# Optimization experiments

Hardware: AMD Instinct MI355X
Metric: run time of the kernel (lower is better)

## Reference

```python
import jax, jax.numpy as jnp
import numpy as np

DIM = 1024
NUM_HEADS = 16
HEAD_DIM = DIM // NUM_HEADS
SCALE = HEAD_DIM ** -0.5


def setup_inputs() -> dict:
    key = jax.random.key(0)
    k1, k2, k3, k4, k5, k6 = jax.random.split(key, 6)
    B, S, L = 4, 8192, 512
    x = jax.random.normal(k1, (B, S, DIM), dtype=jnp.float32)
    latents = jax.random.normal(k2, (B, L, DIM), dtype=jnp.float32)
    # Linear weights stored torch-style as (out_features, in_features)
    w_q = jax.random.normal(k3, (DIM, DIM), dtype=jnp.float32) * (DIM ** -0.5)
    w_kv = jax.random.normal(k4, (2 * DIM, DIM), dtype=jnp.float32) * (DIM ** -0.5)
    w_out = jax.random.normal(k5, (DIM, DIM), dtype=jnp.float32) * (DIM ** -0.5)
    b_out = jax.random.normal(k6, (DIM,), dtype=jnp.float32) * 0.01
    return {"x": x, "latents": latents, "w_q": w_q, "w_kv": w_kv,
            "w_out": w_out, "b_out": b_out}


def reference(x, latents, w_q, w_kv, w_out, b_out):
    B, L, _ = latents.shape
    S = x.shape[1]
    q = latents @ w_q.T                      # (B, L, dim)
    kv = x @ w_kv.T                          # (B, S, 2*dim)
    k, v = jnp.split(kv, 2, axis=-1)         # each (B, S, dim)
    q = q.reshape(B, L, NUM_HEADS, HEAD_DIM)
    k = k.reshape(B, S, NUM_HEADS, HEAD_DIM)
    v = v.reshape(B, S, NUM_HEADS, HEAD_DIM)
    # attention scores: (B, H, L, S)
    attn = jnp.einsum('blhd,bshd->bhls', q, k) * SCALE
    attn = jax.nn.softmax(attn, axis=-1)
    out = jnp.einsum('bhls,bshd->blhd', attn, v)  # (B, L, H, D)
    out = out.reshape(B, L, DIM)
    return out @ w_out.T + b_out
```

## Files before the change

kernel.cpp:

```cpp
#include <hip/hip_runtime.h>
#include <hip/hip_bf16.h>
#include <cstdint>
#include <cstddef>

#define B_ 4
#define S_ 8192
#define L_ 512
#define DIM 1024
#define NUM_HEADS 16
#define HEAD_DIM 64
#define SCHUNK 4096
#define NSEG 2
#define SEGKEYS (SCHUNK / NSEG)
#define SCALE 0.125f
#define L2E 1.44269504088896f
#define F_SC (SCALE * L2E)

typedef __bf16 bf16;
typedef __bf16 bf16x8 __attribute__((ext_vector_type(8)));
typedef float f32x4 __attribute__((ext_vector_type(4)));

#define AS1 __attribute__((address_space(1)))
#define AS3 __attribute__((address_space(3)))
#define GLDS(g, l) __builtin_amdgcn_global_load_lds((const AS1 void*)(g), (AS3 void*)(l), 16, 0, 0)
#define LGKM_FENCE() asm volatile("s_waitcnt lgkmcnt(0)" ::: "memory")
#define MFMA16(a, b, c) __builtin_amdgcn_mfma_f32_16x16x32_bf16((a), (b), (c), 0, 0, 0)

__global__ void detect_dtype(const unsigned int* __restrict__ x, int* __restrict__ flag) {
  int lane = threadIdx.x;
  int cnt = 0;
  for (int i = 0; i < 4; ++i) {
    unsigned int w = x[lane * 4 + i];
    unsigned int e = (w >> 7) & 0xFFu;
    cnt += (e >= 117u && e <= 129u) ? 1 : 0;
  }
  cnt += __shfl_xor(cnt, 1);
  cnt += __shfl_xor(cnt, 2);
  cnt += __shfl_xor(cnt, 4);
  cnt += __shfl_xor(cnt, 8);
  cnt += __shfl_xor(cnt, 16);
  cnt += __shfl_xor(cnt, 32);
  if (lane == 0) *flag = (cnt < 128) ? 1 : 0;
}

template<int REMAP>
__global__ __launch_bounds__(256) void conv_bf16(
    const void* __restrict__ in, bf16* __restrict__ out, int nchunk, int srow0,
    const int* __restrict__ flagp)
{
  const bool f32in = (*flagp != 0);
  for (int c = blockIdx.x * 256 + threadIdx.x; c < nchunk; c += gridDim.x * 256) {
    size_t gc;
    if (REMAP) {
      int r = c >> 7, cc = c & 127;
      gc = ((size_t)((r >> 12) * 8192 + srow0 + (r & 4095)) << 7) + cc;
    } else {
      gc = (size_t)c;
    }
    if (f32in) {
      const f32x4* g = (const f32x4*)in + gc * 2;
      f32x4 lo = g[0], hi = g[1];
      bf16x8 w;
      w[0] = (bf16)lo[0]; w[1] = (bf16)lo[1]; w[2] = (bf16)lo[2]; w[3] = (bf16)lo[3];
      w[4] = (bf16)hi[0]; w[5] = (bf16)hi[1]; w[6] = (bf16)hi[2]; w[7] = (bf16)hi[3];
      *(bf16x8*)(out + (size_t)c * 8) = w;
    } else {
      *(bf16x8*)(out + (size_t)c * 8) = ((const bf16x8*)in)[gc];
    }
  }
}

template<int HAS_BIAS, int DUAL_OUT, int KV_SPLIT, int NBN>
__global__ __launch_bounds__(256) void gemm_nt(
    const bf16* __restrict__ Ap, const bf16* __restrict__ Bwp,
    void* __restrict__ Cp, void* __restrict__ C2p, const void* __restrict__ biasp,
    int M, int N, int K, const int* __restrict__ flagp)
{
  __shared__ __align__(16) bf16 lA[128 * 64];
  __shared__ __align__(16) bf16 lB[128 * 64];
  const int tid = threadIdx.x;
  const int lane = tid & 63, quad = lane >> 4, l16 = lane & 15, wave = tid >> 6;
  const int wm = wave >> 1, wn = wave & 1;
  const int f = blockIdx.x;
  const int xcd = f & 7, sidx = f >> 3;
  const int bn = sidx % NBN;
  const int bm = xcd * (M >> 10) + sidx / NBN;
  const bool f32in = (HAS_BIAS || DUAL_OUT) ? (*flagp != 0) : false;

  f32x4 acc[4][4] = {};
  const int nK = K >> 6;
  for (int kb = 0; kb < nK; ++kb) {
    __syncthreads();
#pragma unroll
    for (int i = 0; i < 4; ++i) {
      int e = i * 256 + tid;
      int row = e >> 3, cp = e & 7, gcp = cp ^ (row & 7);
      const bf16* ga = Ap + (size_t)(bm * 128 + row) * K + kb * 64 + gcp * 8;
      GLDS(ga, lA + e * 8);
      const bf16* gb = Bwp + (size_t)(bn * 128 + row) * K + kb * 64 + gcp * 8;
      GLDS(gb, lB + e * 8);
    }
    __syncthreads();

#pragma unroll
    for (int ks = 0; ks < 2; ++ks) {
      bf16x8 af[4], bfr[4];
#pragma unroll
      for (int t = 0; t < 4; ++t) {
        int rowA = wm * 64 + t * 16 + l16;
        int ca = (ks * 4 + quad) ^ (rowA & 7);
        af[t] = *(const bf16x8*)(lA + rowA * 64 + ca * 8);
        int rowB = wn * 64 + t * 16 + l16;
        int cb = (ks * 4 + quad) ^ (rowB & 7);
        bfr[t] = *(const bf16x8*)(lB + rowB * 64 + cb * 8);
      }
#pragma unroll
      for (int tm = 0; tm < 4; ++tm)
#pragma unroll
        for (int tn = 0; tn < 4; ++tn)
          acc[tm][tn] = MFMA16(af[tm], bfr[tn], acc[tm][tn]);
    }
  }

#pragma unroll
  for (int tn = 0; tn < 4; ++tn) {
    int col = bn * 128 + wn * 64 + tn * 16 + l16;
    float bv = 0.0f;
    if (HAS_BIAS)
      bv = f32in ? ((const float*)biasp)[col] : (float)((const bf16*)biasp)[col];
#pragma unroll
    for (int tm = 0; tm < 4; ++tm) {
#pragma unroll
      for (int r = 0; r < 4; ++r) {
        int rowc = bm * 128 + wm * 64 + tm * 16 + quad * 4 + r;
        float v = acc[tm][tn][r] + bv;
        if (KV_SPLIT) {
          if (col < 1024) ((bf16*)Cp)[(size_t)rowc * 1024 + col] = (bf16)v;
          else            ((bf16*)C2p)[(size_t)rowc * 1024 + col - 1024] = (bf16)v;
        } else if (DUAL_OUT && f32in) {
          ((float*)Cp)[(size_t)rowc * N + col] = v;
        } else {
          ((bf16*)Cp)[(size_t)rowc * N + col] = (bf16)v;
        }
      }
    }
  }
}

template<int FIRST>
__global__ __launch_bounds__(256) void attn_pass(
    const bf16* __restrict__ qb, const bf16* __restrict__ kc, const bf16* __restrict__ vc,
    float* __restrict__ Ost, float* __restrict__ lst)
{
  __shared__ __align__(16) bf16 lK[64 * 64];
  __shared__ __align__(16) bf16 lV[64][72];
  __shared__ __align__(16) bf16 pbuf[4][16][72];
  const int tid = threadIdx.x;
  const int lane = tid & 63, quad = lane >> 4, l16 = lane & 15, wave = tid >> 6;
  const int f = blockIdx.x;
  const int xcd = f & 7, sidx = f >> 3;
  const int lt = sidx & 7, ghi = sidx >> 3;
  const int g = ghi * 8 + xcd;
  const int h = g & 15, bs = g >> 4;
  const int b = bs >> 1, seg = bs & 1;
  const int l0 = lt * 64 + wave * 16;

  const bf16* qbase = qb + (size_t)(b * L_ + l0 + l16) * DIM + h * HEAD_DIM + quad * 8;
  bf16x8 qf0 = *(const bf16x8*)qbase;
  bf16x8 qf1 = *(const bf16x8*)(qbase + 32);

  f32x4 acc[4] = {};
  float lsum[4] = {0.0f, 0.0f, 0.0f, 0.0f};

  const int sbeg = seg * SEGKEYS;
  for (int s0 = sbeg; s0 < sbeg + SEGKEYS; s0 += 64) {
    __syncthreads();
    for (int i = 0; i < 2; ++i) {
      int e = i * 256 + tid;
      int row = e >> 3, cp = e & 7, gcp = cp ^ (row & 7);
      const bf16* gk = kc + (size_t)(b * SCHUNK + s0 + row) * DIM + h * HEAD_DIM + gcp * 8;
      GLDS(gk, lK + e * 8);
    }
    for (int i = 0; i < 2; ++i) {
      int e = i * 256 + tid;
      int row = e >> 3, cc = e & 7;
      bf16x8 vv = *(const bf16x8*)(vc + (size_t)(b * SCHUNK + s0 + row) * DIM + h * HEAD_DIM + cc * 8);
      int pg = (row >> 3) ^ cc;
#pragma unroll
      for (int j = 0; j < 8; ++j)
        lV[cc * 8 + j][pg * 8 + (row & 7)] = vv[j];
    }
    __syncthreads();

    f32x4 sc[4];
#pragma unroll
    for (int kt = 0; kt < 4; ++kt) {
      int rk = kt * 16 + l16;
      int p0c = quad ^ (rk & 7);
      int p1c = (4 + quad) ^ (rk & 7);
      bf16x8 kf0 = *(const bf16x8*)(lK + rk * 64 + p0c * 8);
      bf16x8 kf1 = *(const bf16x8*)(lK + rk * 64 + p1c * 8);
      f32x4 s4 = {};
      s4 = MFMA16(qf0, kf0, s4);
      s4 = MFMA16(qf1, kf1, s4);
      sc[kt] = s4;
    }

#pragma unroll
    for (int r = 0; r < 4; ++r) {
      float a0 = exp2f(fminf(sc[0][r] * F_SC, 40.0f));
      float a1 = exp2f(fminf(sc[1][r] * F_SC, 40.0f));
      float a2 = exp2f(fminf(sc[2][r] * F_SC, 40.0f));
      float a3 = exp2f(fminf(sc[3][r] * F_SC, 40.0f));
      lsum[r] += a0 + a1 + a2 + a3;
      pbuf[wave][quad * 4 + r][l16]      = (bf16)a0;
      pbuf[wave][quad * 4 + r][16 + l16] = (bf16)a1;
      pbuf[wave][quad * 4 + r][32 + l16] = (bf16)a2;
      pbuf[wave][quad * 4 + r][48 + l16] = (bf16)a3;
    }
    LGKM_FENCE();
#pragma unroll
    for (int half = 0; half < 2; ++half) {
      bf16x8 pf = *(const bf16x8*)&pbuf[wave][l16][half * 32 + quad * 8];
#pragma unroll
      for (int t4 = 0; t4 < 4; ++t4) {
        int c = t4 * 16 + l16;
        int pg = (half * 4 + quad) ^ (c >> 3);
        bf16x8 vf = *(const bf16x8*)&lV[c][pg * 8];
        acc[t4] = MFMA16(pf, vf, acc[t4]);
      }
    }
  }

#pragma unroll
  for (int r = 0; r < 4; ++r) {
    lsum[r] += __shfl_xor(lsum[r], 1, 16);
    lsum[r] += __shfl_xor(lsum[r], 2, 16);
    lsum[r] += __shfl_xor(lsum[r], 4, 16);
    lsum[r] += __shfl_xor(lsum[r], 8, 16);
  }

  float* Oseg = Ost + (size_t)seg * (B_ * L_ * DIM);
  float* lseg = lst + (size_t)seg * (B_ * NUM_HEADS * L_);
#pragma unroll
  for (int r = 0; r < 4; ++r) {
    int l = l0 + quad * 4 + r;
    if (l16 == 0) {
      int si = (b * NUM_HEADS + h) * L_ + l;
      if (FIRST) lseg[si] = lsum[r];
      else       lseg[si] += lsum[r];
    }
  }
#pragma unroll
  for (int t4 = 0; t4 < 4; ++t4)
#pragma unroll
    for (int r = 0; r < 4; ++r) {
      int l = l0 + quad * 4 + r;
      size_t oi = (size_t)(b * L_ + l) * DIM + h * HEAD_DIM + t4 * 16 + l16;
      if (FIRST) Oseg[oi] = acc[t4][r];
      else       Oseg[oi] += acc[t4][r];
    }
}

__global__ __launch_bounds__(256) void combine_kernel(
    const float* __restrict__ Ost, const float* __restrict__ lst, bf16* __restrict__ ao)
{
  int idx = (blockIdx.x * 256 + threadIdx.x) * 4;
  int d0 = idx & (DIM - 1);
  int row = idx >> 10;
  int b = row >> 9, l = row & (L_ - 1);
  int h = d0 >> 6;
  int si = (b * NUM_HEADS + h) * L_ + l;
  float lv = lst[si] + lst[B_ * NUM_HEADS * L_ + si];
  float linv = 1.0f / lv;
  f32x4 o0 = *(const f32x4*)(Ost + idx);
  f32x4 o1 = *(const f32x4*)(Ost + (size_t)(B_ * L_ * DIM) + idx);
#pragma unroll
  for (int j = 0; j < 4; ++j)
    ao[idx + j] = (bf16)((o0[j] + o1[j]) * linv);
}

extern "C" void kernel_launch(void* const* d_in, const int* in_sizes, int n_in,
                              void* d_out, int out_size, void* d_ws, size_t ws_size,
                              hipStream_t stream)
{
  (void)in_sizes; (void)n_in; (void)out_size; (void)ws_size;
  const void* x       = d_in[0];
  const void* latents = d_in[1];
  const void* w_q     = d_in[2];
  const void* w_kv    = d_in[3];
  const void* w_out   = d_in[4];
  const void* b_out   = d_in[5];

  char* ws = (char*)d_ws;
  int*   flag  = (int*)ws;
  bf16*  qb    = (bf16*)(ws + ((size_t)1   << 20));
  float* lst   = (float*)(ws + ((size_t)5  << 20));
  bf16*  ao    = (bf16*)(ws + ((size_t)6   << 20));
  float* Ost   = (float*)(ws + ((size_t)10 << 20));
  bf16*  kc    = (bf16*)(ws + ((size_t)26 << 20));
  bf16*  latb  = (bf16*)(ws + ((size_t)26 << 20));
  bf16*  wqb   = (bf16*)(ws + ((size_t)30 << 20));
  bf16*  vc    = (bf16*)(ws + ((size_t)58 << 20));
  bf16*  xcb   = (bf16*)(ws + ((size_t)90 << 20));
  bf16*  wkvb  = (bf16*)(ws + ((size_t)122 << 20));
  bf16*  woutb = (bf16*)(ws + ((size_t)122 << 20));

  detect_dtype<<<1, 64, 0, stream>>>((const unsigned int*)x, flag);

  const int Mx = B_ * SCHUNK;

  conv_bf16<0><<<1024, 256, 0, stream>>>(latents, latb, (B_ * L_ * DIM) / 8, 0, flag);
  conv_bf16<0><<<512,  256, 0, stream>>>(w_q, wqb, (DIM * DIM) / 8, 0, flag);
  conv_bf16<0><<<1024, 256, 0, stream>>>(w_kv, wkvb, (2 * DIM * DIM) / 8, 0, flag);

  gemm_nt<0, 0, 0, 8><<<128, 256, 0, stream>>>(
      latb, wqb, qb, nullptr, nullptr, B_ * L_, DIM, DIM, flag);

  conv_bf16<1><<<2048, 256, 0, stream>>>(x, xcb, (Mx * DIM) / 8, 0, flag);
  gemm_nt<0, 0, 1, 16><<<2048, 256, 0, stream>>>(
      xcb, wkvb, kc, vc, nullptr, Mx, 2048, DIM, flag);
  attn_pass<1><<<1024, 256, 0, stream>>>(qb, kc, vc, Ost, lst);

  conv_bf16<1><<<2048, 256, 0, stream>>>(x, xcb, (Mx * DIM) / 8, SCHUNK, flag);
  gemm_nt<0, 0, 1, 16><<<2048, 256, 0, stream>>>(
      xcb, wkvb, kc, vc, nullptr, Mx, 2048, DIM, flag);
  attn_pass<0><<<1024, 256, 0, stream>>>(qb, kc, vc, Ost, lst);

  conv_bf16<0><<<512, 256, 0, stream>>>(w_out, woutb, (DIM * DIM) / 8, 0, flag);
  combine_kernel<<<(B_ * L_ * DIM / 4) / 256, 256, 0, stream>>>(Ost, lst, ao);

  gemm_nt<1, 1, 0, 8><<<128, 256, 0, stream>>>(
      ao, woutb, d_out, nullptr, b_out, B_ * L_, DIM, DIM, flag);
}
```

Before: 612.8 us.

## Replace KV projection GEMM with 256x256 double-buffered pipelined kernel

Adds a dedicated KV-projection GEMM that uses 256x256 output tiles with 512 threads, double-buffered LDS staging through global_load_lds, interleaved prefetch of the next A and B tiles between MFMA phases, and raised wave priority around the MFMA bursts. It replaces the 128x128 single-buffered generic kernel for the two large x@w_kv^T launches and removes the KV_SPLIT path from the generic kernel. The aim is more data reuse per tile and load latency hidden behind compute. In exchange it uses more LDS and registers, which lowers occupancy, and it launches only 512 blocks.

```diff
diff --git a/kernel.cpp b/kernel.cpp
--- a/kernel.cpp
+++ b/kernel.cpp
@@ -24,6 +24,8 @@
 #define AS3 __attribute__((address_space(3)))
 #define GLDS(g, l) __builtin_amdgcn_global_load_lds((const AS1 void*)(g), (AS3 void*)(l), 16, 0, 0)
 #define LGKM_FENCE() asm volatile("s_waitcnt lgkmcnt(0)" ::: "memory")
+#define VMCNT4() asm volatile("s_waitcnt vmcnt(4)" ::: "memory")
+#define VMCNT0() asm volatile("s_waitcnt vmcnt(0)" ::: "memory")
 #define MFMA16(a, b, c) __builtin_amdgcn_mfma_f32_16x16x32_bf16((a), (b), (c), 0, 0, 0)
 
 __global__ void detect_dtype(const unsigned int* __restrict__ x, int* __restrict__ flag) {
@@ -70,10 +72,10 @@
   }
 }
 
-template<int HAS_BIAS, int DUAL_OUT, int KV_SPLIT, int NBN>
+template<int HAS_BIAS, int DUAL_OUT, int NBN>
 __global__ __launch_bounds__(256) void gemm_nt(
     const bf16* __restrict__ Ap, const bf16* __restrict__ Bwp,
-    void* __restrict__ Cp, void* __restrict__ C2p, const void* __restrict__ biasp,
+    void* __restrict__ Cp, const void* __restrict__ biasp,
     int M, int N, int K, const int* __restrict__ flagp)
 {
   __shared__ __align__(16) bf16 lA[128 * 64];
@@ -134,10 +136,7 @@
       for (int r = 0; r < 4; ++r) {
         int rowc = bm * 128 + wm * 64 + tm * 16 + quad * 4 + r;
         float v = acc[tm][tn][r] + bv;
-        if (KV_SPLIT) {
-          if (col < 1024) ((bf16*)Cp)[(size_t)rowc * 1024 + col] = (bf16)v;
-          else            ((bf16*)C2p)[(size_t)rowc * 1024 + col - 1024] = (bf16)v;
-        } else if (DUAL_OUT && f32in) {
+        if (DUAL_OUT && f32in) {
           ((float*)Cp)[(size_t)rowc * N + col] = v;
         } else {
           ((bf16*)Cp)[(size_t)rowc * N + col] = (bf16)v;
@@ -145,6 +144,113 @@
       }
     }
   }
+}
+
+__global__ __launch_bounds__(512) void gemm_kv_256(
+    const bf16* __restrict__ Ap, const bf16* __restrict__ Bwp,
+    bf16* __restrict__ Cp, bf16* __restrict__ C2p, int M, int K)
+{
+  __shared__ __align__(16) bf16 lA[2][256 * 64];
+  __shared__ __align__(16) bf16 lB[2][256 * 64];
+  const int tid = threadIdx.x;
+  const int lane = tid & 63, quad = lane >> 4, l16 = lane & 15, wave = tid >> 6;
+  const int wm = wave >> 2, wn = wave & 3;
+  const int f = blockIdx.x;
+  const int xcd = f & 7, sidx = f >> 3;
+  const int bn = sidx & 7;
+  const int bm = xcd * ((M >> 8) >> 3) + (sidx >> 3);
+  const int nK = K >> 6;
+
+#define STAGE_A(buf, half, kb) do {                                          \
+  _Pragma("unroll")                                                          \
+  for (int j = 0; j < 2; ++j) {                                              \
+    int e = j * 512 + tid;                                                   \
+    int row = e >> 3, cp = e & 7, gcp = cp ^ (row & 7);                      \
+    const bf16* g = Ap + (size_t)(bm * 256 + (half) * 128 + row) * K         \
+                       + (kb) * 64 + gcp * 8;                                \
+    GLDS(g, &lA[buf][((half) * 128 + row) * 64 + cp * 8]);                   \
+  } } while (0)
+#define STAGE_B(buf, half, kb) do {                                          \
+  _Pragma("unroll")                                                          \
+  for (int j = 0; j < 2; ++j) {                                              \
+    int e = j * 512 + tid;                                                   \
+    int row = e >> 3, cp = e & 7, gcp = cp ^ (row & 7);                      \
+    const bf16* g = Bwp + (size_t)(bn * 256 + (half) * 128 + row) * K        \
+                        + (kb) * 64 + gcp * 8;                               \
+    GLDS(g, &lB[buf][((half) * 128 + row) * 64 + cp * 8]);                   \
+  } } while (0)
+
+  f32x4 acc[8][4] = {};
+
+  STAGE_A(0, 0, 0); STAGE_A(0, 1, 0); STAGE_B(0, 0, 0); STAGE_B(0, 1, 0);
+  if (nK > 1) { STAGE_B(1, 0, 1); STAGE_B(1, 1, 1); VMCNT4(); }
+  else VMCNT0();
+  __builtin_amdgcn_s_barrier();
+
+  for (int t = 0; t < nK; ++t) {
+    const int cur = t & 1;
+    bf16x8 breg[4][2];
+#pragma unroll
+    for (int p = 0; p < 4; ++p) {
+      bf16x8 af[2][2];
+      if (p == 0) {
+#pragma unroll
+        for (int nf = 0; nf < 4; ++nf)
+#pragma unroll
+          for (int ks = 0; ks < 2; ++ks) {
+            int rowB = wn * 64 + nf * 16 + l16;
+            int cb = (ks * 4 + quad) ^ (rowB & 7);
+            breg[nf][ks] = *(const bf16x8*)&lB[cur][rowB * 64 + cb * 8];
+          }
+      }
+#pragma unroll
+      for (int mf2 = 0; mf2 < 2; ++mf2)
+#pragma unroll
+        for (int ks = 0; ks < 2; ++ks) {
+          int rowA = wm * 128 + (p * 2 + mf2) * 16 + l16;
+          int ca = (ks * 4 + quad) ^ (rowA & 7);
+          af[mf2][ks] = *(const bf16x8*)&lA[cur][rowA * 64 + ca * 8];
+        }
+      LGKM_FENCE();
+
+      if (p == 0) { if (t + 1 < nK) STAGE_A(cur ^ 1, 0, t + 1); }
+      else if (p == 1) { if (t + 1 < nK) STAGE_A(cur ^ 1, 1, t + 1); }
+      else if (p == 2) { if (t + 2 < nK) STAGE_B(cur, 0, t + 2); }
+      else             { if (t + 2 < nK) STAGE_B(cur, 1, t + 2); }
+
+      __builtin_amdgcn_s_barrier();
+
+      __builtin_amdgcn_s_setprio(1);
+#pragma unroll
+      for (int mf2 = 0; mf2 < 2; ++mf2)
+#pragma unroll
+        for (int nf = 0; nf < 4; ++nf)
+#pragma unroll
+          for (int ks = 0; ks < 2; ++ks)
+            acc[p * 2 + mf2][nf] = MFMA16(af[mf2][ks], breg[nf][ks], acc[p * 2 + mf2][nf]);
+      __builtin_amdgcn_s_setprio(0);
+    }
+    if (t + 1 < nK) {
+      if (t + 2 < nK) VMCNT4(); else VMCNT0();
+      __builtin_amdgcn_s_barrier();
+    }
+  }
+
+#pragma unroll
+  for (int tn = 0; tn < 4; ++tn) {
+    int col = bn * 256 + wn * 64 + tn * 16 + l16;
+    bf16* outp = (col < 1024) ? Cp : C2p;
+    int ocol = col & 1023;
+#pragma unroll
+    for (int tm = 0; tm < 8; ++tm)
+#pragma unroll
+      for (int r = 0; r < 4; ++r) {
+        int rowc = bm * 256 + wm * 128 + tm * 16 + quad * 4 + r;
+        outp[(size_t)rowc * 1024 + ocol] = (bf16)acc[tm][tn][r];
+      }
+  }
+#undef STAGE_A
+#undef STAGE_B
 }
 
 template<int FIRST>
@@ -314,22 +420,20 @@
   conv_bf16<0><<<512,  256, 0, stream>>>(w_q, wqb, (DIM * DIM) / 8, 0, flag);
   conv_bf16<0><<<1024, 256, 0, stream>>>(w_kv, wkvb, (2 * DIM * DIM) / 8, 0, flag);
 
-  gemm_nt<0, 0, 0, 8><<<128, 256, 0, stream>>>(
-      latb, wqb, qb, nullptr, nullptr, B_ * L_, DIM, DIM, flag);
+  gemm_nt<0, 0, 8><<<128, 256, 0, stream>>>(
+      latb, wqb, qb, nullptr, B_ * L_, DIM, DIM, flag);
 
   conv_bf16<1><<<2048, 256, 0, stream>>>(x, xcb, (Mx * DIM) / 8, 0, flag);
-  gemm_nt<0, 0, 1, 16><<<2048, 256, 0, stream>>>(
-      xcb, wkvb, kc, vc, nullptr, Mx, 2048, DIM, flag);
+  gemm_kv_256<<<512, 512, 0, stream>>>(xcb, wkvb, kc, vc, Mx, DIM);
   attn_pass<1><<<1024, 256, 0, stream>>>(qb, kc, vc, Ost, lst);
 
   conv_bf16<1><<<2048, 256, 0, stream>>>(x, xcb, (Mx * DIM) / 8, SCHUNK, flag);
-  gemm_nt<0, 0, 1, 16><<<2048, 256, 0, stream>>>(
-      xcb, wkvb, kc, vc, nullptr, Mx, 2048, DIM, flag);
+  gemm_kv_256<<<512, 512, 0, stream>>>(xcb, wkvb, kc, vc, Mx, DIM);
   attn_pass<0><<<1024, 256, 0, stream>>>(qb, kc, vc, Ost, lst);
 
   conv_bf16<0><<<512, 256, 0, stream>>>(w_out, woutb, (DIM * DIM) / 8, 0, flag);
   combine_kernel<<<(B_ * L_ * DIM / 4) / 256, 256, 0, stream>>>(Ost, lst, ao);
 
-  gemm_nt<1, 1, 0, 8><<<128, 256, 0, stream>>>(
-      ao, woutb, d_out, nullptr, b_out, B_ * L_, DIM, DIM, flag);
-}
+  gemm_nt<1, 1, 8><<<128, 256, 0, stream>>>(
+      ao, woutb, d_out, b_out, B_ * L_, DIM, DIM, flag);
+}
```

Result: faster. 567.9 us (-7.3%).
